# Performance work log

Measured on AMD Instinct MI355X. Metric: run time of the kernel, lower is better.

The kernel has to match this reference:

```python
import jax, jax.numpy as jnp
import numpy as np

EPS_LN = 1e-6
NUM_HEADS = 3

def ln2d(x, w, b):
    # channels-first layernorm over dim 1 (biased variance), matching LayerNormFunction
    mu = x.mean(1, keepdims=True)
    var = ((x - mu) ** 2).mean(1, keepdims=True)
    y = (x - mu) * jax.lax.rsqrt(var + EPS_LN)
    return w[None, :, None, None] * y + b[None, :, None, None]

def conv1x1(x, w, b):
    # w: (out, in)
    return jnp.einsum('bchw,oc->bohw', x, w) + b[None, :, None, None]

def dwconv3x3(x, w, b):
    # w: (C,1,3,3), depthwise
    C = x.shape[1]
    y = jax.lax.conv_general_dilated(x, w, (1, 1), 'SAME',
        feature_group_count=C, dimension_numbers=('NCHW', 'OIHW', 'NCHW'))
    return y + b[None, :, None, None]

def l2norm(x, eps=1e-12):
    n = jnp.sqrt(jnp.sum(x * x, axis=-1, keepdims=True))
    return x / jnp.maximum(n, eps)

def forward(x, ln1_w, ln1_b, qkv_w, qkv_b, dw_w, dw_b, temp,
            ca_w1, ca_b1, ca_w2, ca_b2, beta, beta2,
            ln2_w, ln2_b, conv4_w, conv4_b, conv5_w, conv5_b, gamma):
    inp = x
    b, c, h, w = x.shape
    xn = ln2d(x, ln1_w, ln1_b)

    # CAB = SE channel attention
    y = xn.mean(axis=(2, 3), keepdims=True)                      # (b,c,1,1)
    y = jax.nn.relu(conv1x1(y, ca_w1, ca_b1))
    y = jax.nn.sigmoid(conv1x1(y, ca_w2, ca_b2))
    outc = xn * y

    # QKV
    qkv = dwconv3x3(conv1x1(xn, qkv_w, qkv_b), dw_w, dw_b)       # (b,3c,h,w)
    q, k, v = jnp.split(qkv, 3, axis=1)
    cph = c // NUM_HEADS
    def to_tokens(t):  # (b,c,h,w) -> (b,head,hw,cph)
        return t.reshape(b, NUM_HEADS, cph, h * w).transpose(0, 1, 3, 2)
    qs = l2norm(to_tokens(q))
    ks = l2norm(to_tokens(k))
    vs = to_tokens(v)

    attns = jnp.einsum('bhnc,bhmc->bhnm', qs, ks) * temp[None]   # (b,head,hw,hw)
    attns = jax.nn.softmax(jax.nn.relu(attns), axis=-1)
    outs = jnp.einsum('bhnm,bhmc->bhnc', attns, vs)              # (b,head,hw,cph)
    outs = outs.transpose(0, 1, 3, 2).reshape(b, c, h, w)

    y1 = inp + outc * beta + outs * beta2

    # gated conv FFN
    f = conv1x1(ln2d(y1, ln2_w, ln2_b), conv4_w, conv4_b)        # (b,2c,h,w)
    f1, f2 = jnp.split(f, 2, axis=1)
    f = conv1x1(f1 * f2, conv5_w, conv5_b)
    return y1 + f * gamma

def setup_inputs() -> dict:
    key = jax.random.key(0)
    ks = jax.random.split(key, 16)
    B, C, H, W = 2, 48, 64, 64
    r = C // 16
    s = 0.05
    return {
        'x': jax.random.normal(ks[0], (B, C, H, W), jnp.float32),
        'ln1_w': jnp.ones((C,), jnp.float32),
        'ln1_b': jnp.zeros((C,), jnp.float32),
        'qkv_w': jax.random.normal(ks[1], (3 * C, C), jnp.float32) * s,
        'qkv_b': jnp.zeros((3 * C,), jnp.float32),
        'dw_w': jax.random.normal(ks[2], (3 * C, 1, 3, 3), jnp.float32) * s,
        'dw_b': jnp.zeros((3 * C,), jnp.float32),
        'temp': jnp.ones((3, 1, 1), jnp.float32),
        'ca_w1': jax.random.normal(ks[3], (r, C), jnp.float32) * s,
        'ca_b1': jnp.zeros((r,), jnp.float32),
        'ca_w2': jax.random.normal(ks[4], (C, r), jnp.float32) * s,
        'ca_b2': jnp.zeros((C,), jnp.float32),
        'beta': jax.random.normal(ks[5], (1, C, 1, 1), jnp.float32) * 0.1,
        'beta2': jax.random.normal(ks[6], (1, C, 1, 1), jnp.float32) * 0.1,
        'ln2_w': jnp.ones((C,), jnp.float32),
        'ln2_b': jnp.zeros((C,), jnp.float32),
        'conv4_w': jax.random.normal(ks[7], (2 * C, C), jnp.float32) * s,
        'conv4_b': jnp.zeros((2 * C,), jnp.float32),
        'conv5_w': jax.random.normal(ks[8], (C, C), jnp.float32) * s,
        'conv5_b': jnp.zeros((C,), jnp.float32),
        'gamma': jax.random.normal(ks[9], (1, C, 1, 1), jnp.float32) * 0.1,
    }

def reference(x, ln1_w, ln1_b, qkv_w, qkv_b, dw_w, dw_b, temp,
              ca_w1, ca_b1, ca_w2, ca_b2, beta, beta2,
              ln2_w, ln2_b, conv4_w, conv4_b, conv5_w, conv5_b, gamma):
    return forward(x, ln1_w, ln1_b, qkv_w, qkv_b, dw_w, dw_b, temp,
                   ca_w1, ca_b1, ca_w2, ca_b2, beta, beta2,
                   ln2_w, ln2_b, conv4_w, conv4_b, conv5_w, conv5_b, gamma)
```

## Files before the change

kernel.cpp:

```cpp
#include <hip/hip_runtime.h>
#include <cstddef>
#include <cmath>

#define BN 2
#define CH 48
#define HW 4096
#define NH 3
#define QC 144
#define RR 3
#define KSPLIT 4
#define NPLANE 17
#define LOG2E 1.4426950408889634f

typedef __attribute__((ext_vector_type(8))) short bf16x8;
typedef __attribute__((ext_vector_type(16))) float f32x16;
typedef __attribute__((ext_vector_type(4))) float f32x4;

constexpr size_t OFF_BP  = 0;
constexpr size_t OFF_QB  = 12288;
constexpr size_t OFF_KB  = OFF_QB + 98304;
constexpr size_t OFF_VT  = OFF_KB + 98304;
constexpr size_t OFF_PART= OFF_VT + 98304 + 1179648;

static __device__ __forceinline__ unsigned cvtpk(float lo, float hi) {
  unsigned r;
  asm("v_cvt_pk_bf16_f32 %0, %1, %2" : "=v"(r) : "v"(lo), "v"(hi));
  return r;
}

static __device__ __forceinline__ float fexp2(float x) {
#if __has_builtin(__builtin_amdgcn_exp2f)
  return __builtin_amdgcn_exp2f(x);
#else
  float r; asm("v_exp_f32 %0, %1" : "=v"(r) : "v"(x)); return r;
#endif
}

__global__ __launch_bounds__(512) void k_front(const float* __restrict__ x,
                                               const float* __restrict__ lw,
                                               const float* __restrict__ lb,
                                               const float* __restrict__ w,
                                               const float* __restrict__ bias,
                                               const float* __restrict__ dww,
                                               const float* __restrict__ dwb,
                                               const float* __restrict__ temp,
                                               ushort* __restrict__ Qb,
                                               ushort* __restrict__ Kb,
                                               ushort* __restrict__ Vtb,
                                               float* __restrict__ bpool) {
  __shared__ float xt1[CH][64];
  __shared__ float qt[3][CH][64];
  __shared__ float red1[8][64], red2[8][64];
  int blk = blockIdx.x;
  int row = blk & 63, bh = blk >> 6;
  int b = bh / NH, h = bh % NH;
  int t = threadIdx.x;
  int px = t & 63, grp = t >> 6;

  for (int r = 0; r < 3; ++r) {
    int yy = row + r - 1;
    if (yy < 0 || yy >= 64) {
      for (int i = t; i < CH*64; i += 512) (&qt[r][0][0])[i] = 0.f;
      __syncthreads();
      continue;
    }
    const float* xb = x + (size_t)b*CH*HW + yy*64 + px;
    float v[6]; float s = 0.f, ss = 0.f;
#pragma unroll
    for (int j = 0; j < 6; ++j) {
      float vv = xb[(size_t)(grp*6 + j)*HW];
      v[j] = vv; s += vv; ss += vv*vv;
    }
    red1[grp][px] = s; red2[grp][px] = ss;
    __syncthreads();
    float stot = 0.f, sstot = 0.f;
#pragma unroll
    for (int i = 0; i < 8; ++i) { stot += red1[i][px]; sstot += red2[i][px]; }
    float mu = stot * (1.f/CH);
    float rs = rsqrtf(sstot*(1.f/CH) - mu*mu + 1e-6f);
#pragma unroll
    for (int j = 0; j < 6; ++j) {
      int c = grp*6 + j;
      xt1[c][px] = lw[c]*((v[j]-mu)*rs) + lb[c];
    }
    __syncthreads();
    if (r == 1 && h == 0 && t < CH) {
      float a = 0.f;
#pragma unroll
      for (int p2 = 0; p2 < 64; ++p2) a += xt1[t][p2];
      bpool[(size_t)(b*64 + row)*CH + t] = a;
    }
    float xv[CH];
#pragma unroll
    for (int ci = 0; ci < CH; ++ci) xv[ci] = xt1[ci][px];
#pragma unroll
    for (int oi = 0; oi < 6; ++oi) {
      int oc = grp*6 + oi;
      int c = __builtin_amdgcn_readfirstlane((oc >> 4)*48 + h*16 + (oc & 15));
      const float* wrow = w + (size_t)c*CH;
      float a = bias[c];
#pragma unroll
      for (int ci = 0; ci < CH; ++ci) a += wrow[ci]*xv[ci];
      qt[r][oc][px] = a;
    }
    __syncthreads();
  }

  int n = row*64 + px;
  float q[2], k[2], vv2[2];
  float sq = 0.f, sk = 0.f;
#pragma unroll
  for (int j = 0; j < 2; ++j) {
    int cc = grp*2 + j;
#pragma unroll
    for (int which = 0; which < 3; ++which) {
      int oc = which*16 + cc;
      int cg = __builtin_amdgcn_readfirstlane(which*48 + h*16 + cc);
      const float* wc = dww + (size_t)cg*9;
      float w0 = wc[0], w1 = wc[1], w2 = wc[2],
            w3 = wc[3], w4 = wc[4], w5 = wc[5],
            w6 = wc[6], w7 = wc[7], w8 = wc[8];
      float a = dwb[cg];
#pragma unroll
      for (int rr = 0; rr < 3; ++rr) {
        float wl = rr==0?w0:(rr==1?w3:w6);
        float wm = rr==0?w1:(rr==1?w4:w7);
        float wr = rr==0?w2:(rr==1?w5:w8);
        float tm = qt[rr][oc][px];
        float tl = (px >= 1)  ? qt[rr][oc][px-1] : 0.f;
        float tr = (px <= 62) ? qt[rr][oc][px+1] : 0.f;
        a += wl*tl + wm*tm + wr*tr;
      }
      if (which == 0)      { q[j] = a;  sq += a*a; }
      else if (which == 1) { k[j] = a;  sk += a*a; }
      else                 vv2[j] = a;
    }
  }
  red1[grp][px] = sq; red2[grp][px] = sk;
  __syncthreads();
  float tsq = 0.f, tsk = 0.f;
#pragma unroll
  for (int i = 0; i < 8; ++i) { tsq += red1[i][px]; tsk += red2[i][px]; }
  float tq = temp[h] * LOG2E / fmaxf(sqrtf(tsq), 1e-12f);
  float ik = 1.f            / fmaxf(sqrtf(tsk), 1e-12f);
  *(uint*)(Qb + ((size_t)bh*HW + n)*16 + grp*2) = cvtpk(q[0]*tq, q[1]*tq);
  *(uint*)(Kb + ((size_t)bh*HW + n)*16 + grp*2) = cvtpk(k[0]*ik, k[1]*ik);
  Vtb[((size_t)bh*16 + grp*2    )*HW + n] = (ushort)(cvtpk(vv2[0], vv2[0]) & 0xffffu);
  Vtb[((size_t)bh*16 + grp*2 + 1)*HW + n] = (ushort)(cvtpk(vv2[1], vv2[1]) & 0xffffu);
}

#define PACK(stv, wbp) do {                                              \
  _Pragma("unroll")                                                      \
  for (int g4 = 0; g4 < 4; ++g4) {                                       \
    float e0 = fmaxf(fexp2((stv)[4*g4+0]), 1.f);                         \
    float e1 = fmaxf(fexp2((stv)[4*g4+1]), 1.f);                         \
    float e2 = fmaxf(fexp2((stv)[4*g4+2]), 1.f);                         \
    float e3 = fmaxf(fexp2((stv)[4*g4+3]), 1.f);                         \
    uint2 pk;                                                            \
    pk.x = cvtpk(e0, e1);                                                \
    pk.y = cvtpk(e2, e3);                                                \
    *(uint2*)((wbp) + wroff + 16*(g4 ^ sw)) = pk;                        \
  } } while (0)

__global__ __launch_bounds__(256) void k_attn(const ushort* __restrict__ Qb,
                                              const ushort* __restrict__ Kb,
                                              const ushort* __restrict__ Vtb,
                                              float* __restrict__ part) {
  __shared__ char smem[4][4096];
  int blk = blockIdx.x;
  int ks = blk & (KSPLIT-1);
  int qt = (blk >> 2) & 31;
  int bh = blk >> 7;
  int lane = threadIdx.x & 63;
  int wid  = threadIdx.x >> 6;
  int l31 = lane & 31;
  int lhi = lane >> 5;
  int qbase = qt*128 + wid*32;

  bf16x8 qf = *(const bf16x8*)(Qb + ((size_t)bh*HW + qbase + l31)*16 + lhi*8);

  const f32x16 z16 = {0,0,0,0,0,0,0,0,0,0,0,0,0,0,0,0};
  const short oneb = (short)0x3f80;
  const bf16x8 ones = {oneb,oneb,oneb,oneb,oneb,oneb,oneb,oneb};
  f32x4 acc0 = {0,0,0,0}, acc1 = {0,0,0,0};
  f32x4 accD0 = {0,0,0,0}, accD1 = {0,0,0,0};
  char* base = &smem[wid][0];
  int qr = lane & 15, gr = lane >> 4;
  int rdoff0 = qr*64 + 16*(gr ^ ((qr>>1)&3));
  int sw = (l31 >> 1) & 3;
  int wroff = l31*64 + 8*lhi;

  const ushort* Kbase = Kb + (size_t)bh*HW*16;
  const ushort* Vbase = Vtb + ((size_t)bh*16 + qr)*HW;
  int kbeg = ks * (HW/KSPLIT);
  constexpr int ITERS = (HW/KSPLIT)/32;

  bf16x8 kf = *(const bf16x8*)(Kbase + (size_t)(kbeg + l31)*16 + lhi*8);
  f32x16 st = __builtin_amdgcn_mfma_f32_32x32x16_bf16(kf, qf, z16, 0, 0, 0);
  bf16x8 kfn = *(const bf16x8*)(Kbase + (size_t)(kbeg + 32 + l31)*16 + lhi*8);
  bf16x8 vfn = *(const bf16x8*)(Vbase + kbeg + 8*gr);
  PACK(st, base);

#pragma unroll 4
  for (int i = 1; i < ITERS; ++i) {
    char* rb = base + ((i-1) & 1)*2048;
    bf16x8 pa0 = *(const bf16x8*)(rb + rdoff0);
    bf16x8 pa1 = *(const bf16x8*)(rb + 1024 + rdoff0);
    __builtin_amdgcn_s_setprio(1);
    f32x16 stn = __builtin_amdgcn_mfma_f32_32x32x16_bf16(kfn, qf, z16, 0, 0, 0);
    kfn = *(const bf16x8*)(Kbase + (size_t)(kbeg + (i+1)*32 + l31)*16 + lhi*8);
    bf16x8 vf = vfn;
    vfn = *(const bf16x8*)(Vbase + kbeg + i*32 + 8*gr);
    acc0  = __builtin_amdgcn_mfma_f32_16x16x32_bf16(pa0, vf, acc0, 0, 0, 0);
    acc1  = __builtin_amdgcn_mfma_f32_16x16x32_bf16(pa1, vf, acc1, 0, 0, 0);
    accD0 = __builtin_amdgcn_mfma_f32_16x16x32_bf16(pa0, ones, accD0, 0, 0, 0);
    accD1 = __builtin_amdgcn_mfma_f32_16x16x32_bf16(pa1, ones, accD1, 0, 0, 0);
    __builtin_amdgcn_s_setprio(0);
    PACK(stn, base + (i & 1)*2048);
  }
  {
    char* rb = base + ((ITERS-1) & 1)*2048;
    bf16x8 pa0 = *(const bf16x8*)(rb + rdoff0);
    bf16x8 pa1 = *(const bf16x8*)(rb + 1024 + rdoff0);
    acc0  = __builtin_amdgcn_mfma_f32_16x16x32_bf16(pa0, vfn, acc0, 0, 0, 0);
    acc1  = __builtin_amdgcn_mfma_f32_16x16x32_bf16(pa1, vfn, acc1, 0, 0, 0);
    accD0 = __builtin_amdgcn_mfma_f32_16x16x32_bf16(pa0, ones, accD0, 0, 0, 0);
    accD1 = __builtin_amdgcn_mfma_f32_16x16x32_bf16(pa1, ones, accD1, 0, 0, 0);
  }

  float* ep = (float*)base;
#pragma unroll
  for (int r = 0; r < 4; ++r) {
    ep[qr*32 + gr*4 + r]      = acc0[r];
    ep[qr*32 + gr*4 + 16 + r] = acc1[r];
  }
  if (qr == 0) {
#pragma unroll
    for (int r = 0; r < 4; ++r) {
      ep[16*32 + gr*4 + r]      = accD0[r];
      ep[16*32 + gr*4 + 16 + r] = accD1[r];
    }
  }
  __syncthreads();
  size_t pb = ((size_t)(ks*6 + bh))*NPLANE;
  for (int i = threadIdx.x; i < 4*32*NPLANE; i += 256) {
    int w = i / (32*NPLANE);
    int rem = i - w*(32*NPLANE);
    int cc = rem >> 5;
    int q = rem & 31;
    part[(pb + cc)*HW + qt*128 + w*32 + q] = ((float*)&smem[w][0])[cc*32 + q];
  }
}

__global__ __launch_bounds__(768) void k_tail(const float* __restrict__ part,
                                              const float* __restrict__ x,
                                              const float* __restrict__ lw1,
                                              const float* __restrict__ lb1,
                                              const float* __restrict__ bpool,
                                              const float* __restrict__ w1,
                                              const float* __restrict__ b1,
                                              const float* __restrict__ w2,
                                              const float* __restrict__ b2,
                                              const float* __restrict__ beta,
                                              const float* __restrict__ beta2,
                                              const float* __restrict__ lw2,
                                              const float* __restrict__ lb2,
                                              const float* __restrict__ w4,
                                              const float* __restrict__ b4,
                                              const float* __restrict__ w5,
                                              const float* __restrict__ b5,
                                              const float* __restrict__ gamma,
                                              float* __restrict__ out) {
  __shared__ float sepm[CH][4];
  __shared__ float pmL[CH];
  __shared__ float yrL[4];
  __shared__ float seL[CH];
  __shared__ float r1[12][64], r2[12][64], r3[12][64], r4[12][64];
  __shared__ float xt[CH][65];
  __shared__ float gt[CH][65];
  int t = threadIdx.x;
  int px = t & 63, w = t >> 6;
  int h = w >> 2;
  int c0 = __builtin_amdgcn_readfirstlane(w * 4);
  int qoff = __builtin_amdgcn_readfirstlane((w & 3) * 4);
  int gp = blockIdx.x*64 + px;
  int b = gp >> 12, n = gp & 4095;
  int bh = b*NH + h;

  if (t < 192) {
    int c = t % CH, j = t / CH;
    const float* bp = bpool + (size_t)(b*64 + j*16)*CH + c;
    float a = 0.f;
#pragma unroll
    for (int i = 0; i < 16; ++i) a += bp[(size_t)i*CH];
    sepm[c][j] = a;
  }
  __syncthreads();
  if (t < CH) pmL[t] = (sepm[t][0]+sepm[t][1]+sepm[t][2]+sepm[t][3]) * (1.f/HW);
  __syncthreads();
  if (t < RR) {
    float a = b1[t];
    for (int c = 0; c < CH; ++c) a += w1[t*CH+c]*pmL[c];
    yrL[t] = fmaxf(a, 0.f);
  }
  __syncthreads();
  if (t < CH) {
    float a = b2[t];
    for (int r = 0; r < RR; ++r) a += w2[t*RR+r]*yrL[r];
    seL[t] = 1.f/(1.f+__expf(-a));
  }

  float acc[4] = {0,0,0,0};
  float den = 0.f;
#pragma unroll
  for (int ks = 0; ks < KSPLIT; ++ks) {
    const float* pl = part + ((size_t)((ks*6+bh)*NPLANE + qoff))*HW + n;
#pragma unroll
    for (int cc = 0; cc < 4; ++cc) acc[cc] += pl[(size_t)cc*HW];
    den += pl[(size_t)(16 - qoff)*HW];
  }
  const float* xp = x + ((size_t)b*CH + c0)*HW + n;
  float xv[4]; float s = 0.f, ssum = 0.f;
#pragma unroll
  for (int cc = 0; cc < 4; ++cc) {
    float vv = xp[(size_t)cc*HW];
    xv[cc] = vv; s += vv; ssum += vv*vv;
  }
  r1[w][px] = s; r2[w][px] = ssum;
  __syncthreads();
  float stot = 0.f, sstot = 0.f;
#pragma unroll
  for (int i = 0; i < 12; ++i) { stot += r1[i][px]; sstot += r2[i][px]; }
  float mu = stot*(1.f/CH);
  float rs = rsqrtf(sstot*(1.f/CH) - mu*mu + 1e-6f);
  float inv = 1.f / den;
  float yv[4]; float s2 = 0.f, ss2 = 0.f;
#pragma unroll
  for (int cc = 0; cc < 4; ++cc) {
    int c = c0 + cc;
    float xnv = lw1[c]*((xv[cc]-mu)*rs) + lb1[c];
    float y = xv[cc] + xnv*seL[c]*beta[c] + acc[cc]*inv*beta2[c];
    yv[cc] = y; s2 += y; ss2 += y*y;
  }
  r3[w][px] = s2; r4[w][px] = ss2;
  __syncthreads();
  float s2t = 0.f, ss2t = 0.f;
#pragma unroll
  for (int i = 0; i < 12; ++i) { s2t += r3[i][px]; ss2t += r4[i][px]; }
  float mu2 = s2t*(1.f/CH);
  float rs2 = rsqrtf(ss2t*(1.f/CH) - mu2*mu2 + 1e-6f);
#pragma unroll
  for (int cc = 0; cc < 4; ++cc) {
    int c = c0 + cc;
    xt[c][px] = lw2[c]*((yv[cc]-mu2)*rs2) + lb2[c];
  }
  __syncthreads();

  float f1[4], f2[4];
#pragma unroll
  for (int j = 0; j < 4; ++j) { f1[j] = b4[c0+j]; f2[j] = b4[CH+c0+j]; }
#pragma unroll 8
  for (int c = 0; c < CH; ++c) {
    float tc = xt[c][px];
#pragma unroll
    for (int j = 0; j < 4; ++j) {
      f1[j] += w4[(size_t)(c0+j)*CH + c] * tc;
      f2[j] += w4[(size_t)(CH+c0+j)*CH + c] * tc;
    }
  }
#pragma unroll
  for (int j = 0; j < 4; ++j) gt[c0+j][px] = f1[j]*f2[j];
  __syncthreads();

  float f5[4];
#pragma unroll
  for (int j = 0; j < 4; ++j) f5[j] = b5[c0+j];
#pragma unroll 8
  for (int c = 0; c < CH; ++c) {
    float gc = gt[c][px];
#pragma unroll
    for (int j = 0; j < 4; ++j) f5[j] += w5[(size_t)(c0+j)*CH + c] * gc;
  }
  float* op = out + ((size_t)b*CH + c0)*HW + n;
#pragma unroll
  for (int j = 0; j < 4; ++j)
    op[(size_t)j*HW] = yv[j] + f5[j]*gamma[c0+j];
}

extern "C" void kernel_launch(void* const* d_in, const int* in_sizes, int n_in,
                              void* d_out, int out_size, void* d_ws, size_t ws_size,
                              hipStream_t stream) {
  const float* x      = (const float*)d_in[0];
  const float* ln1_w  = (const float*)d_in[1];
  const float* ln1_b  = (const float*)d_in[2];
  const float* qkv_w  = (const float*)d_in[3];
  const float* qkv_b  = (const float*)d_in[4];
  const float* dw_w   = (const float*)d_in[5];
  const float* dw_b   = (const float*)d_in[6];
  const float* temp   = (const float*)d_in[7];
  const float* ca_w1  = (const float*)d_in[8];
  const float* ca_b1  = (const float*)d_in[9];
  const float* ca_w2  = (const float*)d_in[10];
  const float* ca_b2  = (const float*)d_in[11];
  const float* beta   = (const float*)d_in[12];
  const float* beta2  = (const float*)d_in[13];
  const float* ln2_w  = (const float*)d_in[14];
  const float* ln2_b  = (const float*)d_in[15];
  const float* conv4_w= (const float*)d_in[16];
  const float* conv4_b= (const float*)d_in[17];
  const float* conv5_w= (const float*)d_in[18];
  const float* conv5_b= (const float*)d_in[19];
  const float* gamma  = (const float*)d_in[20];

  float* ws   = (float*)d_ws;
  float* bp   = ws + OFF_BP;
  ushort* Qb  = (ushort*)(ws + OFF_QB);
  ushort* Kb  = (ushort*)(ws + OFF_KB);
  ushort* Vtb = (ushort*)(ws + OFF_VT);
  float* part = ws + OFF_PART;
  float* out  = (float*)d_out;

  k_front<<<384, 512, 0, stream>>>(x, ln1_w, ln1_b, qkv_w, qkv_b,
                                   dw_w, dw_b, temp, Qb, Kb, Vtb, bp);
  k_attn <<<768, 256, 0, stream>>>(Qb, Kb, Vtb, part);
  k_tail <<<128, 768, 0, stream>>>(part, x, ln1_w, ln1_b, bp,
                                   ca_w1, ca_b1, ca_w2, ca_b2,
                                   beta, beta2, ln2_w, ln2_b,
                                   conv4_w, conv4_b, conv5_w, conv5_b,
                                   gamma, out);
}
```

Measured before the change: 52.47 us.

## Compute front layernorm per thread in registers and split QKV work across waves

Each thread now loads all 48 channels of its pixel and does the layernorm in registers, instead of going through shared xt1 with a cross-wave reduction. The 3 rows x 48 output channels are split into 18-unit slices per wave, so the per-row __syncthreads barriers go away. The pooled-sum output is produced with wave shuffles by the one wave that holds the center row. In exchange, x is reloaded redundantly for rows shared between waves, and the 48-float register array raises register pressure.

Result: slower. 60.32 us (+15.0%).

```diff
diff --git a/kernel.cpp b/kernel.cpp
--- a/kernel.cpp
+++ b/kernel.cpp
@@ -48,7 +48,6 @@
                                                ushort* __restrict__ Kb,
                                                ushort* __restrict__ Vtb,
                                                float* __restrict__ bpool) {
-  __shared__ float xt1[CH][64];
   __shared__ float qt[3][CH][64];
   __shared__ float red1[8][64], red2[8][64];
   int blk = blockIdx.x;
@@ -56,55 +55,53 @@
   int b = bh / NH, h = bh % NH;
   int t = threadIdx.x;
   int px = t & 63, grp = t >> 6;
-
+  int lo = grp*18, hi = lo + 18;
+
+  float xn[CH];
+#pragma unroll
   for (int r = 0; r < 3; ++r) {
+    int rlo = r*48, rhi = rlo + 48;
+    if (lo >= rhi || hi <= rlo) continue;
     int yy = row + r - 1;
-    if (yy < 0 || yy >= 64) {
-      for (int i = t; i < CH*64; i += 512) (&qt[r][0][0])[i] = 0.f;
-      __syncthreads();
-      continue;
-    }
-    const float* xb = x + (size_t)b*CH*HW + yy*64 + px;
-    float v[6]; float s = 0.f, ss = 0.f;
-#pragma unroll
-    for (int j = 0; j < 6; ++j) {
-      float vv = xb[(size_t)(grp*6 + j)*HW];
-      v[j] = vv; s += vv; ss += vv*vv;
-    }
-    red1[grp][px] = s; red2[grp][px] = ss;
-    __syncthreads();
-    float stot = 0.f, sstot = 0.f;
-#pragma unroll
-    for (int i = 0; i < 8; ++i) { stot += red1[i][px]; sstot += red2[i][px]; }
-    float mu = stot * (1.f/CH);
-    float rs = rsqrtf(sstot*(1.f/CH) - mu*mu + 1e-6f);
-#pragma unroll
-    for (int j = 0; j < 6; ++j) {
-      int c = grp*6 + j;
-      xt1[c][px] = lw[c]*((v[j]-mu)*rs) + lb[c];
-    }
-    __syncthreads();
-    if (r == 1 && h == 0 && t < CH) {
-      float a = 0.f;
-#pragma unroll
-      for (int p2 = 0; p2 < 64; ++p2) a += xt1[t][p2];
-      bpool[(size_t)(b*64 + row)*CH + t] = a;
-    }
-    float xv[CH];
-#pragma unroll
-    for (int ci = 0; ci < CH; ++ci) xv[ci] = xt1[ci][px];
-#pragma unroll
-    for (int oi = 0; oi < 6; ++oi) {
-      int oc = grp*6 + oi;
+    bool oob = (yy < 0) || (yy >= 64);
+    if (!oob) {
+      const float* xb = x + (size_t)b*CH*HW + yy*64 + px;
+      float s = 0.f, ss = 0.f;
+#pragma unroll
+      for (int ci = 0; ci < CH; ++ci) {
+        float vv = xb[(size_t)ci*HW];
+        xn[ci] = vv; s += vv; ss += vv*vv;
+      }
+      float mu = s * (1.f/CH);
+      float rs2 = rsqrtf(ss*(1.f/CH) - mu*mu + 1e-6f);
+#pragma unroll
+      for (int ci = 0; ci < CH; ++ci)
+        xn[ci] = lw[ci]*((xn[ci]-mu)*rs2) + lb[ci];
+    }
+    int ub = lo > rlo ? lo : rlo;
+    int ue = hi < rhi ? hi : rhi;
+    for (int u = ub; u < ue; ++u) {
+      int oc = u - rlo;
+      if (oob) { qt[r][oc][px] = 0.f; continue; }
       int c = __builtin_amdgcn_readfirstlane((oc >> 4)*48 + h*16 + (oc & 15));
       const float* wrow = w + (size_t)c*CH;
       float a = bias[c];
 #pragma unroll
-      for (int ci = 0; ci < CH; ++ci) a += wrow[ci]*xv[ci];
+      for (int ci = 0; ci < CH; ++ci) a += wrow[ci]*xn[ci];
       qt[r][oc][px] = a;
     }
-    __syncthreads();
-  }
+  }
+
+  if (h == 0 && grp == 3) {
+#pragma unroll
+    for (int c = 0; c < CH; ++c) {
+      float s = xn[c];
+      s += __shfl_xor(s, 1);  s += __shfl_xor(s, 2);  s += __shfl_xor(s, 4);
+      s += __shfl_xor(s, 8);  s += __shfl_xor(s, 16); s += __shfl_xor(s, 32);
+      if (px == 0) bpool[(size_t)(b*64 + row)*CH + c] = s;
+    }
+  }
+  __syncthreads();
 
   int n = row*64 + px;
   float q[2], k[2], vv2[2];
```
